# Performance work log

Hardware: AMD Instinct MI355X
Metric: run time of the kernel (lower is better)

## Reference

```python
import jax, jax.numpy as jnp
import numpy as np

N_NODES = 100000
INPUT_DIM = 512
OUTPUT_DIM = 128
N_EDGES = 300000


def setup_inputs() -> dict:
    key = jax.random.key(0)
    k1, k2, k3, k4, k5 = jax.random.split(key, 5)
    x = jax.random.normal(k1, (N_NODES, INPUT_DIM), dtype=jnp.float32)
    train_edges = jax.random.randint(k2, (N_EDGES, 2), 0, N_NODES, dtype=jnp.int64)
    train_false_edges = jax.random.randint(k3, (N_EDGES, 2), 0, N_NODES, dtype=jnp.int64)
    # learned params (xavier / kaiming init approximated with uniform fan-based scales)
    limit_w = float(np.sqrt(6.0 / (INPUT_DIM + OUTPUT_DIM)))
    weight = jax.random.uniform(k4, (INPUT_DIM, OUTPUT_DIM), dtype=jnp.float32,
                                minval=-limit_w, maxval=limit_w)
    limit_w3 = float(np.sqrt(6.0 / OUTPUT_DIM) / np.sqrt(2.0))
    weight_three = jax.random.uniform(k5, (OUTPUT_DIM, 1), dtype=jnp.float32,
                                      minval=-limit_w3, maxval=limit_w3)
    return {"x": x, "train_edges": train_edges, "train_false_edges": train_false_edges,
            "weight": weight, "weight_three": weight_three}


def _decode(z, edges, weight_three):
    # gather endpoints, elementwise multiply, matvec against weight_three
    prod = z[edges[:, 0]] * z[edges[:, 1]]  # [E, output_dim]
    return prod @ weight_three               # [E, 1]


def reference(x, train_edges, train_false_edges, weight, weight_three):
    z = x @ weight  # encode: [N, output_dim]
    z1 = _decode(z, train_edges, weight_three)
    z2 = _decode(z, train_false_edges, weight_three)
    return jax.nn.sigmoid(jnp.concatenate((z1, z2), axis=0))
```

## Files before the change

### kernel.cpp

```cpp
#include <hip/hip_runtime.h>
#include <math.h>

#define IN_DIM 512
#define OUT_DIM 128
#define BM 64

typedef __attribute__((ext_vector_type(8))) __bf16 bf16x8;
typedef __attribute__((ext_vector_type(2))) __bf16 bf16x2;
typedef __attribute__((ext_vector_type(4))) float f32x4;
typedef __attribute__((ext_vector_type(2))) float f32x2;

__device__ inline unsigned short f2bf(float f) {
    unsigned u = __float_as_uint(f);
    u += 0x7FFFu + ((u >> 16) & 1u);
    return (unsigned short)(u >> 16);
}

__device__ inline bf16x8 cvt8(const f32x4& lo, const f32x4& hi) {
    bf16x2 p0 = {(__bf16)lo.x, (__bf16)lo.y};
    bf16x2 p1 = {(__bf16)lo.z, (__bf16)lo.w};
    bf16x2 p2 = {(__bf16)hi.x, (__bf16)hi.y};
    bf16x2 p3 = {(__bf16)hi.z, (__bf16)hi.w};
    uint4 u = {__builtin_bit_cast(unsigned, p0), __builtin_bit_cast(unsigned, p1),
               __builtin_bit_cast(unsigned, p2), __builtin_bit_cast(unsigned, p3)};
    return __builtin_bit_cast(bf16x8, u);
}

__device__ inline void gload_lds16(const void* g, void* l) {
    __builtin_amdgcn_global_load_lds(
        (const __attribute__((address_space(1))) void*)g,
        (__attribute__((address_space(3))) void*)l, 16, 0, 0);
}

__global__ void wt2_kernel(const float* __restrict__ w, unsigned short* __restrict__ wt2) {
    int idx = blockIdx.x * 256 + threadIdx.x;
    int k = idx >> 7;
    int n = idx & 127;
    wt2[(((k >> 3) * 128) + n) * 8 + (k & 7)] = f2bf(w[idx]);
}

__global__ __launch_bounds__(256, 4) void gemm_mfma(const float* __restrict__ x,
                                                    const unsigned short* __restrict__ wt2,
                                                    unsigned short* __restrict__ zb,
                                                    int M) {
    __shared__ float sA[8192];
    char* const pAb = (char*)sA;

    const int tid  = threadIdx.x;
    const int lane = tid & 63;
    const int wid  = tid >> 6;
    const int wm   = wid >> 1;
    const int wn   = wid & 1;
    const int block_row = blockIdx.x * BM;

    const int fr  = lane & 15;
    const int fk4 = lane >> 4;

    f32x4 acc[2][4];
#pragma unroll
    for (int i = 0; i < 2; ++i)
#pragma unroll
        for (int j = 0; j < 4; ++j) acc[i][j] = (f32x4){0.f, 0.f, 0.f, 0.f};

    const int s_cb = ((lane & 7) * 16) ^ ((lane >> 3) << 4);
    const char* sbase0;
    const char* sbase1;
    const char* sbase2;
    const char* sbase3;
    {
        int r0 = block_row + wm * 32 + 0 * 8 + (lane >> 3); r0 = (r0 < M) ? r0 : (M - 1);
        int r1 = block_row + wm * 32 + 1 * 8 + (lane >> 3); r1 = (r1 < M) ? r1 : (M - 1);
        int r2 = block_row + wm * 32 + 2 * 8 + (lane >> 3); r2 = (r2 < M) ? r2 : (M - 1);
        int r3 = block_row + wm * 32 + 3 * 8 + (lane >> 3); r3 = (r3 < M) ? r3 : (M - 1);
        sbase0 = (const char*)x + (size_t)r0 * 2048 + s_cb;
        sbase1 = (const char*)x + (size_t)r1 * 2048 + s_cb;
        sbase2 = (const char*)x + (size_t)r2 * 2048 + s_cb;
        sbase3 = (const char*)x + (size_t)r3 * 2048 + s_cb;
    }
    char* const wbase = pAb + wid * 8192;

    const int swz  = (fr & 7) << 4;
    const int cb0  = (fk4 * 32) ^ swz;
    const int cb1  = (fk4 * 32 + 16) ^ swz;
    const int ra0  = fr * 128;
    const int ra1  = (fr + 16) * 128;

    const unsigned short* pb = wt2 + fk4 * 1024 + (wn * 64 + fr) * 8;

    bf16x8 Be0, Be1, Be2, Be3;
    bf16x8 Bo0, Bo1, Bo2, Bo3;

#define LOADB(T, R0, R1, R2, R3)                        \
    R0 = *(const bf16x8*)(pb + (T) * 4096 + 0);         \
    R1 = *(const bf16x8*)(pb + (T) * 4096 + 128);       \
    R2 = *(const bf16x8*)(pb + (T) * 4096 + 256);       \
    R3 = *(const bf16x8*)(pb + (T) * 4096 + 384);

#define STAGE(T, BUF)                                   \
    gload_lds16(sbase0 + (T) * 128, wbase + (BUF) * 4096 + 0);    \
    gload_lds16(sbase1 + (T) * 128, wbase + (BUF) * 4096 + 1024); \
    gload_lds16(sbase2 + (T) * 128, wbase + (BUF) * 4096 + 2048); \
    gload_lds16(sbase3 + (T) * 128, wbase + (BUF) * 4096 + 3072);

#define WAIT8                                                      \
    __builtin_amdgcn_sched_barrier(0);                             \
    asm volatile("s_waitcnt vmcnt(8)" ::: "memory");               \
    __builtin_amdgcn_sched_barrier(0);

#define WAIT0                                                      \
    __builtin_amdgcn_sched_barrier(0);                             \
    asm volatile("s_waitcnt vmcnt(0)" ::: "memory");               \
    __builtin_amdgcn_sched_barrier(0);

#define COMPT(BUF, B0, B1, B2, B3)                                              \
    {                                                                           \
        const char* pT = wbase + (BUF) * 4096;                                  \
        f32x4 lo0 = *(const f32x4*)(pT + ra0 + cb0);                            \
        f32x4 hi0 = *(const f32x4*)(pT + ra0 + cb1);                            \
        f32x4 lo1 = *(const f32x4*)(pT + ra1 + cb0);                            \
        f32x4 hi1 = *(const f32x4*)(pT + ra1 + cb1);                            \
        bf16x8 af0 = cvt8(lo0, hi0);                                            \
        bf16x8 af1 = cvt8(lo1, hi1);                                            \
        acc[0][0] = __builtin_amdgcn_mfma_f32_16x16x32_bf16(af0, B0, acc[0][0], 0, 0, 0); \
        acc[0][1] = __builtin_amdgcn_mfma_f32_16x16x32_bf16(af0, B1, acc[0][1], 0, 0, 0); \
        acc[0][2] = __builtin_amdgcn_mfma_f32_16x16x32_bf16(af0, B2, acc[0][2], 0, 0, 0); \
        acc[0][3] = __builtin_amdgcn_mfma_f32_16x16x32_bf16(af0, B3, acc[0][3], 0, 0, 0); \
        acc[1][0] = __builtin_amdgcn_mfma_f32_16x16x32_bf16(af1, B0, acc[1][0], 0, 0, 0); \
        acc[1][1] = __builtin_amdgcn_mfma_f32_16x16x32_bf16(af1, B1, acc[1][1], 0, 0, 0); \
        acc[1][2] = __builtin_amdgcn_mfma_f32_16x16x32_bf16(af1, B2, acc[1][2], 0, 0, 0); \
        acc[1][3] = __builtin_amdgcn_mfma_f32_16x16x32_bf16(af1, B3, acc[1][3], 0, 0, 0); \
    }

    LOADB(0, Be0, Be1, Be2, Be3);
    STAGE(0, 0);

#pragma unroll
    for (int p = 0; p < 8; ++p) {
        LOADB(2 * p + 1, Bo0, Bo1, Bo2, Bo3);
        STAGE(2 * p + 1, 1);
        WAIT8;
        COMPT(0, Be0, Be1, Be2, Be3);

        if (p < 7) {
            LOADB(2 * p + 2, Be0, Be1, Be2, Be3);
            STAGE(2 * p + 2, 0);
            WAIT8;
        } else {
            WAIT0;
        }
        COMPT(1, Bo0, Bo1, Bo2, Bo3);
    }

#undef LOADB
#undef STAGE
#undef WAIT8
#undef WAIT0
#undef COMPT

    const int crow0 = (lane >> 4) * 4;
    const int ccol  = lane & 15;
#pragma unroll
    for (int mf = 0; mf < 2; ++mf)
#pragma unroll
        for (int r = 0; r < 4; ++r) {
            const int grow = block_row + wm * 32 + mf * 16 + crow0 + r;
            if (grow < M) {
                unsigned short* zr = zb + (size_t)grow * OUT_DIM + wn * 64 + ccol;
#pragma unroll
                for (int nf = 0; nf < 4; ++nf)
                    zr[nf * 16] = f2bf(acc[mf][nf][r]);
            }
        }
}

__device__ inline float dotw3(const uint4& ua, const uint4& ub, const f32x2* w3v) {
    const unsigned pa[4] = {ua.x, ua.y, ua.z, ua.w};
    const unsigned pb[4] = {ub.x, ub.y, ub.z, ub.w};
    f32x2 vv = (f32x2){0.f, 0.f};
#pragma unroll
    for (int i = 0; i < 4; ++i) {
        f32x2 A = (f32x2){__uint_as_float(pa[i] << 16),
                          __uint_as_float(pa[i] & 0xFFFF0000u)};
        f32x2 B = (f32x2){__uint_as_float(pb[i] << 16),
                          __uint_as_float(pb[i] & 0xFFFF0000u)};
        vv += (A * B) * w3v[i];
    }
    return vv.x + vv.y;
}

__global__ __launch_bounds__(256) void decode_kernel(const unsigned short* __restrict__ zb,
                                                     const int* __restrict__ e1,
                                                     const int* __restrict__ e2,
                                                     const float* __restrict__ w3,
                                                     float* __restrict__ out,
                                                     int E1, int E2) {
    const int tid  = threadIdx.x;
    const int lane = tid & 63;
    const int sub  = lane & 15;
    const int sg   = lane >> 4;
    const int Etot = E1 + E2;
    const int nq   = (Etot + 3) >> 2;

    f32x2 w3v[4];
    {
        const float4 wlo = *(const float4*)(w3 + sub * 8);
        const float4 whi = *(const float4*)(w3 + sub * 8 + 4);
        w3v[0] = (f32x2){wlo.x, wlo.y};
        w3v[1] = (f32x2){wlo.z, wlo.w};
        w3v[2] = (f32x2){whi.x, whi.y};
        w3v[3] = (f32x2){whi.z, whi.w};
    }

    const int wave = blockIdx.x * 4 + (tid >> 6);
    const int S    = gridDim.x * 4;

    for (int q = wave; q < nq; q += 2 * S) {
        const int q2    = q + S;
        const bool has2 = (q2 < nq);

        const int e_a = q * 4 + sg;
        const int e_b = has2 ? (q2 * 4 + sg) : e_a;
        const int ca  = min(e_a, Etot - 1);
        const int cb  = min(e_b, Etot - 1);

        const int2 ia = (ca < E1) ? ((const int2*)e1)[ca] : ((const int2*)e2)[ca - E1];
        const int2 ib = (cb < E1) ? ((const int2*)e1)[cb] : ((const int2*)e2)[cb - E1];

        const uint4 a1 = *(const uint4*)(zb + (size_t)ia.x * OUT_DIM + sub * 8);
        const uint4 b1 = *(const uint4*)(zb + (size_t)ia.y * OUT_DIM + sub * 8);
        const uint4 a2 = *(const uint4*)(zb + (size_t)ib.x * OUT_DIM + sub * 8);
        const uint4 b2 = *(const uint4*)(zb + (size_t)ib.y * OUT_DIM + sub * 8);

        float v1 = dotw3(a1, b1, w3v);
        float v2 = dotw3(a2, b2, w3v);

        v1 += __shfl_xor(v1, 8);  v2 += __shfl_xor(v2, 8);
        v1 += __shfl_xor(v1, 4);  v2 += __shfl_xor(v2, 4);
        v1 += __shfl_xor(v1, 2);  v2 += __shfl_xor(v2, 2);
        v1 += __shfl_xor(v1, 1);  v2 += __shfl_xor(v2, 1);

        if (sub == 0) {
            if (e_a < Etot) out[e_a] = 1.f / (1.f + __expf(-v1));
            if (has2 && e_b < Etot) out[e_b] = 1.f / (1.f + __expf(-v2));
        }
    }
}

extern "C" void kernel_launch(void* const* d_in, const int* in_sizes, int n_in,
                              void* d_out, int out_size, void* d_ws, size_t ws_size,
                              hipStream_t stream) {
    const float* x  = (const float*)d_in[0];
    const int*   e1 = (const int*)d_in[1];
    const int*   e2 = (const int*)d_in[2];
    const float* w  = (const float*)d_in[3];
    const float* w3 = (const float*)d_in[4];

    float* out = (float*)d_out;

    const int M  = in_sizes[0] / IN_DIM;
    const int E1 = in_sizes[1] / 2;
    const int E2 = in_sizes[2] / 2;

    unsigned short* zbuf = (unsigned short*)d_ws;
    unsigned short* wt2  = zbuf + (size_t)M * OUT_DIM;

    wt2_kernel<<<(IN_DIM * OUT_DIM) / 256, 256, 0, stream>>>(w, wt2);
    gemm_mfma<<<(M + BM - 1) / BM, 256, 0, stream>>>(x, wt2, zbuf, M);
    decode_kernel<<<2048, 256, 0, stream>>>(zbuf, e1, e2, w3, out, E1, E2);
}
```

Measured before the change: 89.21 us.

## Triple-buffer GEMM staging and transpose MFMA operands for vectorized bf16 stores

Replaces the double-buffered LDS staging of x tiles with a three-deep pipeline, keeping two tiles of loads in flight while computing one. LDS per block grows and occupancy hint drops from 4 to 3 blocks per CU. MFMA operands are swapped so each lane holds four consecutive output columns, which lets the epilogue write packed 8-byte bf16 stores instead of scalar 2-byte stores. The extra in-flight B registers raise register pressure.

Result: slower. 91.26 us (+2.3%).

```diff
diff --git a/kernel.cpp b/kernel.cpp
--- a/kernel.cpp
+++ b/kernel.cpp
@@ -14,6 +14,9 @@
     unsigned u = __float_as_uint(f);
     u += 0x7FFFu + ((u >> 16) & 1u);
     return (unsigned short)(u >> 16);
+}
+__device__ inline unsigned pack2f(float a, float b) {
+    return (unsigned)f2bf(a) | ((unsigned)f2bf(b) << 16);
 }
 
 __device__ inline bf16x8 cvt8(const f32x4& lo, const f32x4& hi) {
@@ -39,11 +42,11 @@
     wt2[(((k >> 3) * 128) + n) * 8 + (k & 7)] = f2bf(w[idx]);
 }
 
-__global__ __launch_bounds__(256, 4) void gemm_mfma(const float* __restrict__ x,
+__global__ __launch_bounds__(256, 3) void gemm_mfma(const float* __restrict__ x,
                                                     const unsigned short* __restrict__ wt2,
                                                     unsigned short* __restrict__ zb,
                                                     int M) {
-    __shared__ float sA[8192];
+    __shared__ float sA[12288];
     char* const pAb = (char*)sA;
 
     const int tid  = threadIdx.x;
@@ -77,7 +80,7 @@
         sbase2 = (const char*)x + (size_t)r2 * 2048 + s_cb;
         sbase3 = (const char*)x + (size_t)r3 * 2048 + s_cb;
     }
-    char* const wbase = pAb + wid * 8192;
+    char* const wbase = pAb + wid * 12288;
 
     const int swz  = (fr & 7) << 4;
     const int cb0  = (fk4 * 32) ^ swz;
@@ -87,32 +90,26 @@
 
     const unsigned short* pb = wt2 + fk4 * 1024 + (wn * 64 + fr) * 8;
 
-    bf16x8 Be0, Be1, Be2, Be3;
-    bf16x8 Bo0, Bo1, Bo2, Bo3;
-
-#define LOADB(T, R0, R1, R2, R3)                        \
-    R0 = *(const bf16x8*)(pb + (T) * 4096 + 0);         \
-    R1 = *(const bf16x8*)(pb + (T) * 4096 + 128);       \
-    R2 = *(const bf16x8*)(pb + (T) * 4096 + 256);       \
-    R3 = *(const bf16x8*)(pb + (T) * 4096 + 384);
-
-#define STAGE(T, BUF)                                   \
-    gload_lds16(sbase0 + (T) * 128, wbase + (BUF) * 4096 + 0);    \
-    gload_lds16(sbase1 + (T) * 128, wbase + (BUF) * 4096 + 1024); \
-    gload_lds16(sbase2 + (T) * 128, wbase + (BUF) * 4096 + 2048); \
+    bf16x8 Ba0, Ba1, Ba2, Ba3;
+    bf16x8 Bb0, Bb1, Bb2, Bb3;
+    bf16x8 Bc0, Bc1, Bc2, Bc3;
+
+#define ISSUE(T, BUF, R0, R1, R2, R3)                                \
+    R0 = *(const bf16x8*)(pb + (T) * 4096 + 0);                      \
+    R1 = *(const bf16x8*)(pb + (T) * 4096 + 128);                    \
+    R2 = *(const bf16x8*)(pb + (T) * 4096 + 256);                    \
+    R3 = *(const bf16x8*)(pb + (T) * 4096 + 384);                    \
+    gload_lds16(sbase0 + (T) * 128, wbase + (BUF) * 4096 + 0);       \
+    gload_lds16(sbase1 + (T) * 128, wbase + (BUF) * 4096 + 1024);    \
+    gload_lds16(sbase2 + (T) * 128, wbase + (BUF) * 4096 + 2048);    \
     gload_lds16(sbase3 + (T) * 128, wbase + (BUF) * 4096 + 3072);
 
-#define WAIT8                                                      \
-    __builtin_amdgcn_sched_barrier(0);                             \
-    asm volatile("s_waitcnt vmcnt(8)" ::: "memory");               \
+#define WAITN(N)                                                     \
+    __builtin_amdgcn_sched_barrier(0);                               \
+    asm volatile("s_waitcnt vmcnt(" #N ")" ::: "memory");            \
     __builtin_amdgcn_sched_barrier(0);
 
-#define WAIT0                                                      \
-    __builtin_amdgcn_sched_barrier(0);                             \
-    asm volatile("s_waitcnt vmcnt(0)" ::: "memory");               \
-    __builtin_amdgcn_sched_barrier(0);
-
-#define COMPT(BUF, B0, B1, B2, B3)                                              \
+#define COMP(BUF, B0, B1, B2, B3)                                               \
     {                                                                           \
         const char* pT = wbase + (BUF) * 4096;                                  \
         f32x4 lo0 = *(const f32x4*)(pT + ra0 + cb0);                            \
@@ -121,56 +118,56 @@
         f32x4 hi1 = *(const f32x4*)(pT + ra1 + cb1);                            \
         bf16x8 af0 = cvt8(lo0, hi0);                                            \
         bf16x8 af1 = cvt8(lo1, hi1);                                            \
-        acc[0][0] = __builtin_amdgcn_mfma_f32_16x16x32_bf16(af0, B0, acc[0][0], 0, 0, 0); \
-        acc[0][1] = __builtin_amdgcn_mfma_f32_16x16x32_bf16(af0, B1, acc[0][1], 0, 0, 0); \
-        acc[0][2] = __builtin_amdgcn_mfma_f32_16x16x32_bf16(af0, B2, acc[0][2], 0, 0, 0); \
-        acc[0][3] = __builtin_amdgcn_mfma_f32_16x16x32_bf16(af0, B3, acc[0][3], 0, 0, 0); \
-        acc[1][0] = __builtin_amdgcn_mfma_f32_16x16x32_bf16(af1, B0, acc[1][0], 0, 0, 0); \
-        acc[1][1] = __builtin_amdgcn_mfma_f32_16x16x32_bf16(af1, B1, acc[1][1], 0, 0, 0); \
-        acc[1][2] = __builtin_amdgcn_mfma_f32_16x16x32_bf16(af1, B2, acc[1][2], 0, 0, 0); \
-        acc[1][3] = __builtin_amdgcn_mfma_f32_16x16x32_bf16(af1, B3, acc[1][3], 0, 0, 0); \
-    }
-
-    LOADB(0, Be0, Be1, Be2, Be3);
-    STAGE(0, 0);
-
-#pragma unroll
-    for (int p = 0; p < 8; ++p) {
-        LOADB(2 * p + 1, Bo0, Bo1, Bo2, Bo3);
-        STAGE(2 * p + 1, 1);
-        WAIT8;
-        COMPT(0, Be0, Be1, Be2, Be3);
-
-        if (p < 7) {
-            LOADB(2 * p + 2, Be0, Be1, Be2, Be3);
-            STAGE(2 * p + 2, 0);
-            WAIT8;
-        } else {
-            WAIT0;
-        }
-        COMPT(1, Bo0, Bo1, Bo2, Bo3);
-    }
-
-#undef LOADB
-#undef STAGE
-#undef WAIT8
-#undef WAIT0
-#undef COMPT
-
-    const int crow0 = (lane >> 4) * 4;
-    const int ccol  = lane & 15;
-#pragma unroll
-    for (int mf = 0; mf < 2; ++mf)
-#pragma unroll
-        for (int r = 0; r < 4; ++r) {
-            const int grow = block_row + wm * 32 + mf * 16 + crow0 + r;
-            if (grow < M) {
-                unsigned short* zr = zb + (size_t)grow * OUT_DIM + wn * 64 + ccol;
-#pragma unroll
-                for (int nf = 0; nf < 4; ++nf)
-                    zr[nf * 16] = f2bf(acc[mf][nf][r]);
+        acc[0][0] = __builtin_amdgcn_mfma_f32_16x16x32_bf16(B0, af0, acc[0][0], 0, 0, 0); \
+        acc[0][1] = __builtin_amdgcn_mfma_f32_16x16x32_bf16(B1, af0, acc[0][1], 0, 0, 0); \
+        acc[0][2] = __builtin_amdgcn_mfma_f32_16x16x32_bf16(B2, af0, acc[0][2], 0, 0, 0); \
+        acc[0][3] = __builtin_amdgcn_mfma_f32_16x16x32_bf16(B3, af0, acc[0][3], 0, 0, 0); \
+        acc[1][0] = __builtin_amdgcn_mfma_f32_16x16x32_bf16(B0, af1, acc[1][0], 0, 0, 0); \
+        acc[1][1] = __builtin_amdgcn_mfma_f32_16x16x32_bf16(B1, af1, acc[1][1], 0, 0, 0); \
+        acc[1][2] = __builtin_amdgcn_mfma_f32_16x16x32_bf16(B2, af1, acc[1][2], 0, 0, 0); \
+        acc[1][3] = __builtin_amdgcn_mfma_f32_16x16x32_bf16(B3, af1, acc[1][3], 0, 0, 0); \
+    }
+
+    ISSUE(0, 0, Ba0, Ba1, Ba2, Ba3);
+    ISSUE(1, 1, Bb0, Bb1, Bb2, Bb3);
+    ISSUE(2, 2, Bc0, Bc1, Bc2, Bc3);
+    WAITN(16); COMP(0, Ba0, Ba1, Ba2, Ba3); ISSUE(3, 0, Ba0, Ba1, Ba2, Ba3);
+    WAITN(16); COMP(1, Bb0, Bb1, Bb2, Bb3); ISSUE(4, 1, Bb0, Bb1, Bb2, Bb3);
+    WAITN(16); COMP(2, Bc0, Bc1, Bc2, Bc3); ISSUE(5, 2, Bc0, Bc1, Bc2, Bc3);
+    WAITN(16); COMP(0, Ba0, Ba1, Ba2, Ba3); ISSUE(6, 0, Ba0, Ba1, Ba2, Ba3);
+    WAITN(16); COMP(1, Bb0, Bb1, Bb2, Bb3); ISSUE(7, 1, Bb0, Bb1, Bb2, Bb3);
+    WAITN(16); COMP(2, Bc0, Bc1, Bc2, Bc3); ISSUE(8, 2, Bc0, Bc1, Bc2, Bc3);
+    WAITN(16); COMP(0, Ba0, Ba1, Ba2, Ba3); ISSUE(9, 0, Ba0, Ba1, Ba2, Ba3);
+    WAITN(16); COMP(1, Bb0, Bb1, Bb2, Bb3); ISSUE(10, 1, Bb0, Bb1, Bb2, Bb3);
+    WAITN(16); COMP(2, Bc0, Bc1, Bc2, Bc3); ISSUE(11, 2, Bc0, Bc1, Bc2, Bc3);
+    WAITN(16); COMP(0, Ba0, Ba1, Ba2, Ba3); ISSUE(12, 0, Ba0, Ba1, Ba2, Ba3);
+    WAITN(16); COMP(1, Bb0, Bb1, Bb2, Bb3); ISSUE(13, 1, Bb0, Bb1, Bb2, Bb3);
+    WAITN(16); COMP(2, Bc0, Bc1, Bc2, Bc3); ISSUE(14, 2, Bc0, Bc1, Bc2, Bc3);
+    WAITN(16); COMP(0, Ba0, Ba1, Ba2, Ba3); ISSUE(15, 0, Ba0, Ba1, Ba2, Ba3);
+    WAITN(16); COMP(1, Bb0, Bb1, Bb2, Bb3);
+    WAITN(8);  COMP(2, Bc0, Bc1, Bc2, Bc3);
+    WAITN(0);  COMP(0, Ba0, Ba1, Ba2, Ba3);
+
+#undef ISSUE
+#undef WAITN
+#undef COMP
+
+    const int cm  = lane & 15;
+    const int cn0 = (lane >> 4) * 4;
+#pragma unroll
+    for (int mf = 0; mf < 2; ++mf) {
+        const int grow = block_row + wm * 32 + mf * 16 + cm;
+        if (grow < M) {
+            unsigned short* zr = zb + (size_t)grow * OUT_DIM + wn * 64 + cn0;
+#pragma unroll
+            for (int nf = 0; nf < 4; ++nf) {
+                uint2 u;
+                u.x = pack2f(acc[mf][nf][0], acc[mf][nf][1]);
+                u.y = pack2f(acc[mf][nf][2], acc[mf][nf][3]);
+                *(uint2*)(zr + nf * 16) = u;
             }
         }
+    }
 }
 
 __device__ inline float dotw3(const uint4& ua, const uint4& ub, const f32x2* w3v) {
```
